# Optimization experiments

Hardware: AMD Instinct MI355X
Metric: run time of the kernel (lower is better)

The kernel has to match this reference:

```python
import jax, jax.numpy as jnp
import numpy as np

N = 4096      # nnode
F = 128       # feature_dim
E = 64        # embed_dim
P_EDGE = 0.01 # edge probability (~41 avg degree)
NEG = -9e15
ALPHA = 0.2   # leaky relu slope


def _xavier(key, shape):
    lim = float(np.sqrt(6.0 / (shape[0] + shape[1])))
    return jax.random.uniform(key, shape, minval=-lim, maxval=lim, dtype=jnp.float32)


def setup_inputs() -> dict:
    key = jax.random.key(0)
    ks = jax.random.split(key, 14)
    features = jax.random.normal(ks[0], (N, F), dtype=jnp.float32)
    eye = jnp.eye(N, dtype=jnp.float32)

    def make_adj(k):
        a = (jax.random.uniform(k, (N, N)) < P_EDGE).astype(jnp.float32)
        return jnp.maximum(a, eye)  # self loop so no empty rows

    return {
        "features": features,
        "geo_adj": make_adj(ks[1]),
        "forward_adj": make_adj(ks[2]),
        "backward_adj": make_adj(ks[3]),
        "weight": _xavier(ks[4], (E, F)),
        "Wf": _xavier(ks[5], (F, E)),
        "af1": jax.random.normal(ks[6], (E,), dtype=jnp.float32) * 0.1,
        "af2": jax.random.normal(ks[7], (E,), dtype=jnp.float32) * 0.1,
        "Wb": _xavier(ks[8], (F, E)),
        "ab1": jax.random.normal(ks[9], (E,), dtype=jnp.float32) * 0.1,
        "ab2": jax.random.normal(ks[10], (E,), dtype=jnp.float32) * 0.1,
        "Wg": _xavier(ks[11], (F, E)),
        "ag1": jax.random.normal(ks[12], (E,), dtype=jnp.float32) * 0.1,
        "ag2": jax.random.normal(ks[13], (E,), dtype=jnp.float32) * 0.1,
    }


def _mean_neighbors(adj, feat):
    # pre_weight: row-normalized neighbor averaging, (N,N) @ (N,F)
    deg = jnp.clip(jnp.sum(adj, axis=1, keepdims=True), 1.0, None)
    return (adj @ feat) / deg


def _attention(feat, mask_feat, adj, W, a1, a2):
    # GAT-style additive attention with masked softmax over neighbors
    h = feat @ W        # (N, E)
    hm = mask_feat @ W  # (N, E)
    e = jax.nn.leaky_relu((h @ a1)[:, None] + (hm @ a2)[None, :], negative_slope=ALPHA)  # (N, N)
    e = jnp.where(adj > 0, e, NEG)
    return jax.nn.softmax(e, axis=1)  # (N, N)


def reference(features, geo_adj, forward_adj, backward_adj, weight,
              Wf, af1, af2, Wb, ab1, ab2, Wg, ag1, ag2):
    t = features  # (N, F)
    mask_f = _mean_neighbors(forward_adj, t)
    mask_b = _mean_neighbors(backward_adj, t)
    mask_g = _mean_neighbors(geo_adj, t)

    w_f = _attention(t, mask_f, forward_adj, Wf, af1, af2)
    w_b = _attention(t, mask_b, backward_adj, Wb, ab1, ab2)
    w_g = _attention(t, mask_g, geo_adj, Wg, ag1, ag2)

    # get_mask_matrix_i/_j broadcast-mul + sum(1) == attn @ t (or attn.T @ t)
    x = weight @ t.T                  # (E, N)
    x_fwd = weight @ (w_f @ t).T      # mask_matrix_i
    x_bwd = weight @ (w_b.T @ t).T    # mask_matrix_j (transposed)
    x_geo = weight @ (w_g @ t).T      # mask_matrix_i

    return jnp.concatenate([x, x_fwd, x_bwd, x_geo], axis=0)  # (4E, N)
```

## Files before the change

### kernel.cpp

```cpp
#include <hip/hip_runtime.h>

#define NN 4096
#define FF 128
#define EE 64

typedef unsigned short u16;
typedef unsigned long long u64;

__device__ __forceinline__ float lrelu(float x) { return x > 0.f ? x : 0.2f * x; }

__global__ void k_prep(const float* __restrict__ Wf, const float* __restrict__ af1, const float* __restrict__ af2,
                       const float* __restrict__ Wb, const float* __restrict__ ab1, const float* __restrict__ ab2,
                       const float* __restrict__ Wg, const float* __restrict__ ag1, const float* __restrict__ ag2,
                       float* __restrict__ v6)
{
    const float* Ws[3]  = {Wf, Wb, Wg};
    const float* a1s[3] = {af1, ab1, ag1};
    const float* a2s[3] = {af2, ab2, ag2};
    int vi = blockIdx.x, f = threadIdx.x, dd = vi >> 1;
    const float* a = (vi & 1) ? a2s[dd] : a1s[dd];
    const float* W = Ws[dd] + (size_t)f * EE;
    float s = 0.f;
    #pragma unroll 8
    for (int e = 0; e < EE; ++e) s += W[e] * a[e];
    v6[vi * FF + f] = s;
}

__global__ void k_feat(const float* __restrict__ t, const float* __restrict__ weight,
                       const float* __restrict__ v6,
                       float* __restrict__ u, float* __restrict__ s1, float* __restrict__ p,
                       float* __restrict__ out, int* __restrict__ ccnt)
{
    __shared__ __attribute__((aligned(16))) float tt[FF];
    __shared__ float vv[6 * FF];
    int n = blockIdx.x, tid = threadIdx.x;
    if (n < 16) ccnt[n * 256 + tid] = 0;
    if (tid < FF) tt[tid] = t[(size_t)n * FF + tid];
    for (int idx = tid; idx < 6 * FF; idx += 256) vv[idx] = v6[idx];
    __syncthreads();
    int e = tid >> 2, part = tid & 3;
    const float4* w4 = reinterpret_cast<const float4*>(weight + (size_t)e * FF + part * 32);
    const float4* t4 = reinterpret_cast<const float4*>(tt + part * 32);
    float s = 0.f;
    #pragma unroll
    for (int q8 = 0; q8 < 8; ++q8) {
        float4 w = w4[q8]; float4 x = t4[q8];
        s += w.x * x.x + w.y * x.y + w.z * x.z + w.w * x.w;
    }
    s += __shfl_xor(s, 1); s += __shfl_xor(s, 2);
    if (part == 0) {
        u[(size_t)n * EE + e] = s;
        out[(size_t)e * NN + n] = s;
    }
    if (tid < 64) {
        float t0 = tt[tid], t1 = tt[64 + tid];
        for (int vi = 0; vi < 6; ++vi) {
            float x = t0 * vv[vi * FF + tid] + t1 * vv[vi * FF + 64 + tid];
            for (int off = 32; off; off >>= 1) x += __shfl_xor(x, off);
            if (tid == 0) {
                int dd = vi >> 1;
                if (vi & 1) p[dd * NN + n] = x; else s1[dd * NN + n] = x;
            }
        }
    }
}

__global__ __launch_bounds__(256, 4)
void k_scan(const float* __restrict__ Af, const float* __restrict__ Ab, const float* __restrict__ Ag,
            const float* __restrict__ p,
            u16* __restrict__ csr, int* __restrict__ cnt, float* __restrict__ s2,
            u16* __restrict__ csc, int* __restrict__ ccnt, int stride)
{
    int wid = threadIdx.x >> 6, lane = threadIdx.x & 63;
    int gr = blockIdx.x * 4 + wid;
    int d = gr >> 12, r = gr & (NN - 1);
    const float* A = d == 0 ? Af : (d == 1 ? Ab : Ag);
    const float4* row4 = reinterpret_cast<const float4*>(A + (size_t)r * NN);
    const float* pd = p + d * NN;

    u64 mask = 0ull;
    #pragma unroll
    for (int j = 0; j < 16; ++j) {
        float4 L = row4[j * 64 + lane];
        unsigned mm = (L.x != 0.f ? 1u : 0u) | (L.y != 0.f ? 2u : 0u) |
                      (L.z != 0.f ? 4u : 0u) | (L.w != 0.f ? 8u : 0u);
        mask |= ((u64)mm) << (j * 4);
    }

    int lc = __popcll(mask);
    int sc = lc;
    for (int off = 1; off < 64; off <<= 1) {
        int o = __shfl_up(sc, off);
        if (lane >= off) sc += o;
    }
    int total = __shfl(sc, 63);
    int pos = sc - lc;
    u16* crow = csr + (size_t)gr * stride;
    float q = 0.f;
    u64 m = mask;
    while (m) {
        int b = __ffsll(m) - 1;
        m &= m - 1;
        int col = ((b >> 2) << 8) + (lane << 2) + (b & 3);
        if (pos < stride) crow[pos] = (u16)col;
        pos++;
        q += pd[col];
        if (d == 1) {
            int cp = atomicAdd(&ccnt[col], 1);
            if (cp < stride) csc[(size_t)col * stride + cp] = (u16)r;
        }
    }
    for (int off = 32; off; off >>= 1) q += __shfl_xor(q, off);
    if (lane == 0) {
        cnt[gr] = total;
        s2[gr] = q / fmaxf((float)total, 1.f);
    }
}

__global__ void k_zb(const float* __restrict__ s1, const float* __restrict__ s2,
                     const u16* __restrict__ csr, const int* __restrict__ cnt, int stride,
                     float* __restrict__ Zb)
{
    int tid = threadIdx.x, wave = tid >> 6, lane = tid & 63;
    int j = blockIdx.x * 4 + wave;
    int gr = NN + j;
    int nnz = min(cnt[gr], stride);
    const u16* crow = csr + (size_t)gr * stride;
    float s1j = s1[gr];
    const float* s2b = s2 + NN;
    float z = 0.f;
    if (lane < nnz)      z += __expf(lrelu(s1j + s2b[crow[lane]]));
    if (lane + 64 < nnz) z += __expf(lrelu(s1j + s2b[crow[lane + 64]]));
    for (int off = 32; off; off >>= 1) z += __shfl_xor(z, off);
    if (lane == 0) Zb[j] = z;
}

__global__ __launch_bounds__(256, 4)
void k_out(const float* __restrict__ u,
           const float* __restrict__ s1, const float* __restrict__ s2,
           const float* __restrict__ Zb,
           const u16* __restrict__ csr, const int* __restrict__ cnt,
           const u16* __restrict__ csc, const int* __restrict__ ccnt, int stride,
           float* __restrict__ out)
{
    int wid = threadIdx.x >> 6, lane = threadIdx.x & 63;
    int gr = blockIdx.x * 4 + wid;
    int d = gr >> 12, i = gr & (NN - 1);
    int nnz;
    int c0v = 0, c1v = 0;
    float w0v = 0.f, w1v = 0.f;
    if (d == 1) {
        nnz = min(ccnt[i], stride);
        const u16* cc = csc + (size_t)i * stride;
        float s2i = s2[NN + i];
        if (lane < nnz)      { int j = cc[lane];      c0v = j; w0v = __expf(lrelu(s1[NN + j] + s2i)) / Zb[j]; }
        if (lane + 64 < nnz) { int j = cc[lane + 64]; c1v = j; w1v = __expf(lrelu(s1[NN + j] + s2i)) / Zb[j]; }
    } else {
        nnz = min(cnt[gr], stride);
        const u16* crow = csr + (size_t)gr * stride;
        float s1i = s1[gr];
        const float* s2d = s2 + d * NN;
        float z = 0.f;
        if (lane < nnz)      { int c = crow[lane];      c0v = c; w0v = __expf(lrelu(s1i + s2d[c])); z += w0v; }
        if (lane + 64 < nnz) { int c = crow[lane + 64]; c1v = c; w1v = __expf(lrelu(s1i + s2d[c])); z += w1v; }
        for (int off = 32; off; off >>= 1) z += __shfl_xor(z, off);
        float invz = z > 0.f ? 1.f / z : 0.f;
        w0v *= invz; w1v *= invz;
    }
    float a0 = 0.f, a1 = 0.f;
    int n0 = nnz < 64 ? nnz : 64;
    int k = 0;
    for (; k + 1 < n0; k += 2) {
        int ca = __shfl(c0v, k), cb = __shfl(c0v, k + 1);
        float wa = __shfl(w0v, k), wb = __shfl(w0v, k + 1);
        a0 += wa * u[(size_t)ca * EE + lane];
        a1 += wb * u[(size_t)cb * EE + lane];
    }
    if (k < n0)
        a0 += __shfl(w0v, k) * u[(size_t)__shfl(c0v, k) * EE + lane];
    int n1 = nnz - 64;
    k = 0;
    for (; k + 1 < n1; k += 2) {
        int ca = __shfl(c1v, k), cb = __shfl(c1v, k + 1);
        float wa = __shfl(w1v, k), wb = __shfl(w1v, k + 1);
        a0 += wa * u[(size_t)ca * EE + lane];
        a1 += wb * u[(size_t)cb * EE + lane];
    }
    if (k < n1)
        a0 += __shfl(w1v, k) * u[(size_t)__shfl(c1v, k) * EE + lane];
    int base = 64 + (d << 6);
    out[(size_t)(base + lane) * NN + i] = a0 + a1;
}

extern "C" void kernel_launch(void* const* d_in, const int* in_sizes, int n_in,
                              void* d_out, int out_size, void* d_ws, size_t ws_size,
                              hipStream_t stream)
{
    const float* t   = (const float*)d_in[0];
    const float* Ag  = (const float*)d_in[1];
    const float* Af  = (const float*)d_in[2];
    const float* Ab  = (const float*)d_in[3];
    const float* W   = (const float*)d_in[4];
    const float* Wf  = (const float*)d_in[5];
    const float* af1 = (const float*)d_in[6];
    const float* af2 = (const float*)d_in[7];
    const float* Wb  = (const float*)d_in[8];
    const float* ab1 = (const float*)d_in[9];
    const float* ab2 = (const float*)d_in[10];
    const float* Wg  = (const float*)d_in[11];
    const float* ag1 = (const float*)d_in[12];
    const float* ag2 = (const float*)d_in[13];
    float* out = (float*)d_out;

    float* ws = (float*)d_ws;
    float* v6  = ws;
    float* s1  = v6 + 6 * FF;
    float* p   = s1 + 3 * NN;
    float* s2  = p + 3 * NN;
    float* Zb  = s2 + 3 * NN;
    float* u   = Zb + NN;
    int*   cnt  = (int*)(u + (size_t)NN * EE);
    int*   ccnt = cnt + 3 * NN;
    u16*   csr  = (u16*)(ccnt + NN);

    size_t base_bytes = ((char*)csr) - ((char*)d_ws);
    int stride = 128;
    if (base_bytes + (size_t)4 * NN * 128 * 2 > ws_size) stride = 96;
    if (base_bytes + (size_t)4 * NN * 96 * 2 > ws_size)  stride = 64;
    u16* csc = csr + (size_t)3 * NN * stride;

    k_prep<<<6, 128, 0, stream>>>(Wf, af1, af2, Wb, ab1, ab2, Wg, ag1, ag2, v6);
    k_feat<<<NN, 256, 0, stream>>>(t, W, v6, u, s1, p, out, ccnt);
    k_scan<<<3 * NN / 4, 256, 0, stream>>>(Af, Ab, Ag, p, csr, cnt, s2, csc, ccnt, stride);
    k_zb<<<NN / 4, 256, 0, stream>>>(s1, s2, csr, cnt, stride, Zb);
    k_out<<<3 * NN / 4, 256, 0, stream>>>(u, s1, s2, Zb, csr, cnt, csc, ccnt, stride, out);
}
```

Before: 269.9 us.

## Batch 16 nodes per block in feat and out kernels with coalesced transposed stores

k_feat now handles 16 nodes per block. It stages the weight matrix and the node rows in padded shared memory, then writes the transposed output through a shared buffer so that global stores are contiguous. k_out likewise handles 16 rows per block and stages results in shared memory, turning strided column writes into coalesced row writes. This targets the uncoalesced scattered writes to the (4E, N) output and the per-node reloading of weight. The cost is fewer blocks and more shared memory per block, which lowers occupancy.

```diff
diff --git a/kernel.cpp b/kernel.cpp
--- a/kernel.cpp
+++ b/kernel.cpp
@@ -26,43 +26,62 @@
     v6[vi * FF + f] = s;
 }
 
-__global__ void k_feat(const float* __restrict__ t, const float* __restrict__ weight,
-                       const float* __restrict__ v6,
-                       float* __restrict__ u, float* __restrict__ s1, float* __restrict__ p,
-                       float* __restrict__ out, int* __restrict__ ccnt)
-{
-    __shared__ __attribute__((aligned(16))) float tt[FF];
+__global__ __launch_bounds__(256)
+void k_feat(const float* __restrict__ t, const float* __restrict__ weight,
+            const float* __restrict__ v6,
+            float* __restrict__ u, float* __restrict__ s1, float* __restrict__ p,
+            float* __restrict__ out, int* __restrict__ ccnt)
+{
+    __shared__ float ww[64 * 129];
+    __shared__ float tt[16 * 130];
     __shared__ float vv[6 * FF];
-    int n = blockIdx.x, tid = threadIdx.x;
-    if (n < 16) ccnt[n * 256 + tid] = 0;
-    if (tid < FF) tt[tid] = t[(size_t)n * FF + tid];
-    for (int idx = tid; idx < 6 * FF; idx += 256) vv[idx] = v6[idx];
+    __shared__ float uacc[64 * 17];
+    int b = blockIdx.x, tid = threadIdx.x;
+    int n0 = b * 16;
+    if (b < 16) ccnt[b * 256 + tid] = 0;
+    const float4* w4 = reinterpret_cast<const float4*>(weight);
+    for (int i = tid; i < 2048; i += 256) {
+        float4 v = w4[i];
+        int fi = i * 4, e = fi >> 7, q = fi & 127;
+        float* dst = &ww[e * 129 + q];
+        dst[0] = v.x; dst[1] = v.y; dst[2] = v.z; dst[3] = v.w;
+    }
+    const float4* t4 = reinterpret_cast<const float4*>(t + (size_t)n0 * FF);
+    for (int i = tid; i < 512; i += 256) {
+        float4 v = t4[i];
+        int fi = i * 4, nd = fi >> 7, q = fi & 127;
+        float* dst = &tt[nd * 130 + q];
+        dst[0] = v.x; dst[1] = v.y; dst[2] = v.z; dst[3] = v.w;
+    }
+    for (int i = tid; i < 6 * FF; i += 256) vv[i] = v6[i];
     __syncthreads();
-    int e = tid >> 2, part = tid & 3;
-    const float4* w4 = reinterpret_cast<const float4*>(weight + (size_t)e * FF + part * 32);
-    const float4* t4 = reinterpret_cast<const float4*>(tt + part * 32);
-    float s = 0.f;
-    #pragma unroll
-    for (int q8 = 0; q8 < 8; ++q8) {
-        float4 w = w4[q8]; float4 x = t4[q8];
-        s += w.x * x.x + w.y * x.y + w.z * x.z + w.w * x.w;
-    }
-    s += __shfl_xor(s, 1); s += __shfl_xor(s, 2);
-    if (part == 0) {
-        u[(size_t)n * EE + e] = s;
-        out[(size_t)e * NN + n] = s;
-    }
-    if (tid < 64) {
-        float t0 = tt[tid], t1 = tt[64 + tid];
+    int g = tid >> 6, lane = tid & 63;
+    for (int k = 0; k < 4; ++k) {
+        int nd = g * 4 + k;
+        const float* trow = &tt[nd * 130];
+        const float* wrow = &ww[lane * 129];
+        float acc = 0.f;
+        #pragma unroll 16
+        for (int q = 0; q < 128; ++q) acc += wrow[q] * trow[q];
+        u[(size_t)(n0 + nd) * EE + lane] = acc;
+        uacc[lane * 17 + nd] = acc;
+        float t0 = trow[lane], t1 = trow[64 + lane];
         for (int vi = 0; vi < 6; ++vi) {
-            float x = t0 * vv[vi * FF + tid] + t1 * vv[vi * FF + 64 + tid];
+            float x = t0 * vv[vi * FF + lane] + t1 * vv[vi * FF + 64 + lane];
             for (int off = 32; off; off >>= 1) x += __shfl_xor(x, off);
-            if (tid == 0) {
+            if (lane == 0) {
                 int dd = vi >> 1;
-                if (vi & 1) p[dd * NN + n] = x; else s1[dd * NN + n] = x;
+                if (vi & 1) p[dd * NN + n0 + nd] = x; else s1[dd * NN + n0 + nd] = x;
             }
         }
     }
+    __syncthreads();
+    int e = tid >> 2, io = (tid & 3) * 4;
+    float* orow = out + (size_t)e * NN + n0 + io;
+    orow[0] = uacc[e * 17 + io];
+    orow[1] = uacc[e * 17 + io + 1];
+    orow[2] = uacc[e * 17 + io + 2];
+    orow[3] = uacc[e * 17 + io + 3];
 }
 
 __global__ __launch_bounds__(256, 4)
@@ -135,7 +154,7 @@
     if (lane == 0) Zb[j] = z;
 }
 
-__global__ __launch_bounds__(256, 4)
+__global__ __launch_bounds__(256)
 void k_out(const float* __restrict__ u,
            const float* __restrict__ s1, const float* __restrict__ s2,
            const float* __restrict__ Zb,
@@ -143,53 +162,66 @@
            const u16* __restrict__ csc, const int* __restrict__ ccnt, int stride,
            float* __restrict__ out)
 {
+    __shared__ float oacc[16 * 66];
+    int gr0 = blockIdx.x * 16;
+    int d = gr0 >> 12, i0 = gr0 & (NN - 1);
     int wid = threadIdx.x >> 6, lane = threadIdx.x & 63;
-    int gr = blockIdx.x * 4 + wid;
-    int d = gr >> 12, i = gr & (NN - 1);
-    int nnz;
-    int c0v = 0, c1v = 0;
-    float w0v = 0.f, w1v = 0.f;
-    if (d == 1) {
-        nnz = min(ccnt[i], stride);
-        const u16* cc = csc + (size_t)i * stride;
-        float s2i = s2[NN + i];
-        if (lane < nnz)      { int j = cc[lane];      c0v = j; w0v = __expf(lrelu(s1[NN + j] + s2i)) / Zb[j]; }
-        if (lane + 64 < nnz) { int j = cc[lane + 64]; c1v = j; w1v = __expf(lrelu(s1[NN + j] + s2i)) / Zb[j]; }
-    } else {
-        nnz = min(cnt[gr], stride);
-        const u16* crow = csr + (size_t)gr * stride;
-        float s1i = s1[gr];
-        const float* s2d = s2 + d * NN;
-        float z = 0.f;
-        if (lane < nnz)      { int c = crow[lane];      c0v = c; w0v = __expf(lrelu(s1i + s2d[c])); z += w0v; }
-        if (lane + 64 < nnz) { int c = crow[lane + 64]; c1v = c; w1v = __expf(lrelu(s1i + s2d[c])); z += w1v; }
-        for (int off = 32; off; off >>= 1) z += __shfl_xor(z, off);
-        float invz = z > 0.f ? 1.f / z : 0.f;
-        w0v *= invz; w1v *= invz;
-    }
-    float a0 = 0.f, a1 = 0.f;
-    int n0 = nnz < 64 ? nnz : 64;
-    int k = 0;
-    for (; k + 1 < n0; k += 2) {
-        int ca = __shfl(c0v, k), cb = __shfl(c0v, k + 1);
-        float wa = __shfl(w0v, k), wb = __shfl(w0v, k + 1);
-        a0 += wa * u[(size_t)ca * EE + lane];
-        a1 += wb * u[(size_t)cb * EE + lane];
-    }
-    if (k < n0)
-        a0 += __shfl(w0v, k) * u[(size_t)__shfl(c0v, k) * EE + lane];
-    int n1 = nnz - 64;
-    k = 0;
-    for (; k + 1 < n1; k += 2) {
-        int ca = __shfl(c1v, k), cb = __shfl(c1v, k + 1);
-        float wa = __shfl(w1v, k), wb = __shfl(w1v, k + 1);
-        a0 += wa * u[(size_t)ca * EE + lane];
-        a1 += wb * u[(size_t)cb * EE + lane];
-    }
-    if (k < n1)
-        a0 += __shfl(w1v, k) * u[(size_t)__shfl(c1v, k) * EE + lane];
+    for (int k = 0; k < 4; ++k) {
+        int lr = k * 4 + wid;
+        int i = i0 + lr;
+        int gr = gr0 + lr;
+        int nnz;
+        int c0v = 0, c1v = 0;
+        float w0v = 0.f, w1v = 0.f;
+        if (d == 1) {
+            nnz = min(ccnt[i], stride);
+            const u16* cc = csc + (size_t)i * stride;
+            float s2i = s2[NN + i];
+            if (lane < nnz)      { int j = cc[lane];      c0v = j; w0v = __expf(lrelu(s1[NN + j] + s2i)) / Zb[j]; }
+            if (lane + 64 < nnz) { int j = cc[lane + 64]; c1v = j; w1v = __expf(lrelu(s1[NN + j] + s2i)) / Zb[j]; }
+        } else {
+            nnz = min(cnt[gr], stride);
+            const u16* crow = csr + (size_t)gr * stride;
+            float s1i = s1[gr];
+            const float* s2d = s2 + d * NN;
+            float z = 0.f;
+            if (lane < nnz)      { int c = crow[lane];      c0v = c; w0v = __expf(lrelu(s1i + s2d[c])); z += w0v; }
+            if (lane + 64 < nnz) { int c = crow[lane + 64]; c1v = c; w1v = __expf(lrelu(s1i + s2d[c])); z += w1v; }
+            for (int off = 32; off; off >>= 1) z += __shfl_xor(z, off);
+            float invz = z > 0.f ? 1.f / z : 0.f;
+            w0v *= invz; w1v *= invz;
+        }
+        float a0 = 0.f, a1 = 0.f;
+        int n0 = nnz < 64 ? nnz : 64;
+        int kk = 0;
+        for (; kk + 1 < n0; kk += 2) {
+            int ca = __shfl(c0v, kk), cb = __shfl(c0v, kk + 1);
+            float wa = __shfl(w0v, kk), wb = __shfl(w0v, kk + 1);
+            a0 += wa * u[(size_t)ca * EE + lane];
+            a1 += wb * u[(size_t)cb * EE + lane];
+        }
+        if (kk < n0)
+            a0 += __shfl(w0v, kk) * u[(size_t)__shfl(c0v, kk) * EE + lane];
+        int n1 = nnz - 64;
+        kk = 0;
+        for (; kk + 1 < n1; kk += 2) {
+            int ca = __shfl(c1v, kk), cb = __shfl(c1v, kk + 1);
+            float wa = __shfl(w1v, kk), wb = __shfl(w1v, kk + 1);
+            a0 += wa * u[(size_t)ca * EE + lane];
+            a1 += wb * u[(size_t)cb * EE + lane];
+        }
+        if (kk < n1)
+            a0 += __shfl(w1v, kk) * u[(size_t)__shfl(c1v, kk) * EE + lane];
+        oacc[lr * 66 + lane] = a0 + a1;
+    }
+    __syncthreads();
+    int e = threadIdx.x >> 2, io = (threadIdx.x & 3) * 4;
     int base = 64 + (d << 6);
-    out[(size_t)(base + lane) * NN + i] = a0 + a1;
+    float* orow = out + (size_t)(base + e) * NN + i0 + io;
+    orow[0] = oacc[(io    ) * 66 + e];
+    orow[1] = oacc[(io + 1) * 66 + e];
+    orow[2] = oacc[(io + 2) * 66 + e];
+    orow[3] = oacc[(io + 3) * 66 + e];
 }
 
 extern "C" void kernel_launch(void* const* d_in, const int* in_sizes, int n_in,
@@ -230,8 +262,8 @@
     u16* csc = csr + (size_t)3 * NN * stride;
 
     k_prep<<<6, 128, 0, stream>>>(Wf, af1, af2, Wb, ab1, ab2, Wg, ag1, ag2, v6);
-    k_feat<<<NN, 256, 0, stream>>>(t, W, v6, u, s1, p, out, ccnt);
+    k_feat<<<NN / 16, 256, 0, stream>>>(t, W, v6, u, s1, p, out, ccnt);
     k_scan<<<3 * NN / 4, 256, 0, stream>>>(Af, Ab, Ag, p, csr, cnt, s2, csc, ccnt, stride);
     k_zb<<<NN / 4, 256, 0, stream>>>(s1, s2, csr, cnt, stride, Zb);
-    k_out<<<3 * NN / 4, 256, 0, stream>>>(u, s1, s2, Zb, csr, cnt, csc, ccnt, stride, out);
-}
+    k_out<<<3 * NN / 16, 256, 0, stream>>>(u, s1, s2, Zb, csr, cnt, csc, ccnt, stride, out);
+}
```

Result: no change. 270.5 us (median of 2 runs) (+0.2%).
